# Kernel optimization log

Measured on AMD Instinct MI355X. Metric: run time of the kernel, lower is better.

Reference implementation:

```python
import jax, jax.numpy as jnp
import numpy as np

NUM_GROUPS = 8
EPS = 1e-5


def setup_inputs() -> dict:
    key = jax.random.key(0)
    ks = jax.random.split(key, 7)
    b, c, h, w = 4, 256, 64, 64
    x = jax.random.normal(ks[0], (b, c, h, w), dtype=jnp.float32)
    gamma = jnp.ones((c,), dtype=jnp.float32)
    beta = jnp.zeros((c,), dtype=jnp.float32)
    # 1x1 convs stored as [out_ch, in_ch] matrices
    w_qkv = jax.random.normal(ks[1], (3 * c, c), dtype=jnp.float32) * (1.0 / np.sqrt(c))
    b_qkv = jax.random.normal(ks[2], (3 * c,), dtype=jnp.float32) * 0.01
    # NOTE: original zero-inits proj; use small random weights so the op is non-trivial
    w_proj = jax.random.normal(ks[3], (c, c), dtype=jnp.float32) * (1.0 / np.sqrt(c))
    b_proj = jax.random.normal(ks[4], (c,), dtype=jnp.float32) * 0.01
    return {"x": x, "gamma": gamma, "beta": beta, "w_qkv": w_qkv,
            "b_qkv": b_qkv, "w_proj": w_proj, "b_proj": b_proj}


def _group_norm(x, gamma, beta):
    b, c, h, w = x.shape
    xg = x.reshape(b, NUM_GROUPS, c // NUM_GROUPS, h, w)
    mean = jnp.mean(xg, axis=(2, 3, 4), keepdims=True)
    var = jnp.var(xg, axis=(2, 3, 4), keepdims=True)
    xg = (xg - mean) * jax.lax.rsqrt(var + EPS)
    x = xg.reshape(b, c, h, w)
    return x * gamma[None, :, None, None] + beta[None, :, None, None]


def reference(x, gamma, beta, w_qkv, b_qkv, w_proj, b_proj):
    b, c, h, w = x.shape
    n = h * w
    residual = x
    xn = _group_norm(x, gamma, beta)
    # 1x1 conv qkv: [b, 3c, h, w]
    qkv = jnp.einsum('bchw,oc->bohw', xn, w_qkv) + b_qkv[None, :, None, None]
    q, k, v = jnp.split(qkv, 3, axis=1)
    q = q.reshape(b, c, n).transpose(0, 2, 1)   # [b, n, c]
    k = k.reshape(b, c, n)                       # [b, c, n]
    v = v.reshape(b, c, n).transpose(0, 2, 1)   # [b, n, c]
    scale = 1.0 / jnp.sqrt(jnp.asarray(c, dtype=x.dtype))
    attn = jnp.einsum('bic,bcj->bij', q, k) * scale    # [b, n, n]
    attn = jax.nn.softmax(attn, axis=-1)
    out = jnp.einsum('bij,bjc->bic', attn, v)          # [b, n, c]
    out = out.transpose(0, 2, 1).reshape(b, c, h, w)
    out = jnp.einsum('bchw,oc->bohw', out, w_proj) + b_proj[None, :, None, None]
    return out + residual
```

## Files before the change

### kernel.cpp

```cpp
#include <hip/hip_runtime.h>
#include <math.h>

#define BB   4
#define CC   256
#define NN   4096
#define GG   8
#define CPG  32
#define EPSV 1e-5f
#define SCALE 0.0625f
#define NSPLIT 4
#define PSTR 40

typedef __attribute__((ext_vector_type(8))) short bf16x8;
typedef __attribute__((ext_vector_type(4))) float f32x4;

struct alignas(8) us4 { unsigned short x, y, z, w; };

static __device__ __forceinline__ unsigned short f2bf(float f) {
    union { float f; unsigned int u; } a; a.f = f;
    unsigned int r = a.u + 0x7fffu + ((a.u >> 16) & 1u);
    return (unsigned short)(r >> 16);
}
static __device__ __forceinline__ void async16(const unsigned short* g, unsigned short* l) {
    __builtin_amdgcn_global_load_lds(
        (const __attribute__((address_space(1))) unsigned int*)g,
        (__attribute__((address_space(3))) unsigned int*)l,
        16, 0, 0);
}


__global__ __launch_bounds__(256) void prep_kernel(
    const float* __restrict__ x, const float* __restrict__ w_qkv,
    const float* __restrict__ w_proj, float* __restrict__ partials,
    unsigned short* __restrict__ wbf)
{
    const int tid = threadIdx.x;
    if (blockIdx.x >= 256) {
        int idx = ((blockIdx.x - 256)*256 + tid) * 4;
        float4 v;
        if (idx < 196608) v = *(const float4*)(w_qkv + idx);
        else              v = *(const float4*)(w_proj + (idx - 196608));
        us4 h = { f2bf(v.x), f2bf(v.y), f2bf(v.z), f2bf(v.w) };
        int o = idx >> 8, c = idx & 255;
        size_t dst = ((size_t)((o >> 4)*8 + (c >> 5)))*512
                   + ((((c & 31) >> 3))*16 + (o & 15))*8 + (c & 7);
        *(us4*)(wbf + dst) = h;
        return;
    }
    const int bg = blockIdx.x >> 3, slice = blockIdx.x & 7;
    const float4* base = (const float4*)(x + (size_t)bg*CPG*NN + slice*16384);
    float s = 0.f, sq = 0.f;
    for (int i = tid; i < 4096; i += 256) {
        float4 v = base[i];
        s  += v.x + v.y + v.z + v.w;
        sq += v.x*v.x + v.y*v.y + v.z*v.z + v.w*v.w;
    }
    __shared__ float ls[256], lq[256];
    ls[tid] = s; lq[tid] = sq;
    __syncthreads();
    for (int off = 128; off > 0; off >>= 1) {
        if (tid < off) { ls[tid] += ls[tid+off]; lq[tid] += lq[tid+off]; }
        __syncthreads();
    }
    if (tid == 0) { partials[blockIdx.x*2] = ls[0]; partials[blockIdx.x*2+1] = lq[0]; }
}

__global__ __launch_bounds__(256) void norm_t_kernel(
    const float* __restrict__ x, const float* __restrict__ gamma,
    const float* __restrict__ beta, const float* __restrict__ partials,
    unsigned short* __restrict__ xnT)
{
    const int n0 = blockIdx.x * 64;
    const int c0 = blockIdx.y * 64;
    const int b  = blockIdx.z;
    const int tid = threadIdx.x;
    __shared__ unsigned short T[64*68];
    __shared__ float ssc[64], ssh[64];
    if (tid < 64) {
        int c = c0 + tid;
        int bg = b*GG + (c >> 5);
        float s = 0.f, sq = 0.f;
        for (int i = 0; i < 8; i++) {
            s  += partials[(bg*8 + i)*2];
            sq += partials[(bg*8 + i)*2 + 1];
        }
        const float cnt = (float)(CPG*NN);
        float mean = s / cnt;
        float var  = sq / cnt - mean*mean;
        float rstd = rsqrtf(var + EPSV);
        float g = gamma[c], be = beta[c];
        ssc[tid] = rstd*g;
        ssh[tid] = be - mean*rstd*g;
    }
    __syncthreads();
    {
        int cl = tid >> 4, n4 = tid & 15;
        for (int i = 0; i < 4; i++) {
            int c = cl + i*16;
            float4 v = *(const float4*)(x + ((size_t)(b*CC + c0 + c))*NN + n0 + n4*4);
            float sc = ssc[c], sh = ssh[c];
            T[(n4*4+0)*68 + c] = f2bf(v.x*sc + sh);
            T[(n4*4+1)*68 + c] = f2bf(v.y*sc + sh);
            T[(n4*4+2)*68 + c] = f2bf(v.z*sc + sh);
            T[(n4*4+3)*68 + c] = f2bf(v.w*sc + sh);
        }
    }
    __syncthreads();
    {
        int nl = tid >> 3, cs = tid & 7;
        for (int i = 0; i < 2; i++) {
            int n = nl + i*32;
            int gg = (b*NN + n0 + n) >> 4;
            int kk = (c0 >> 5) + (cs >> 2);
            size_t dst = ((size_t)(gg*8 + kk))*512 + ((cs & 3)*16 + (n & 15))*8;
            *(bf16x8*)(xnT + dst) = *(const bf16x8*)&T[n*68 + cs*8];
        }
    }
}

__global__ __launch_bounds__(256, 3) void qkv_mfma_kernel(
    const unsigned short* __restrict__ xnT, const unsigned short* __restrict__ wbf,
    const float* __restrict__ b_qkv,
    unsigned short* __restrict__ qsw, unsigned short* __restrict__ ksw,
    unsigned short* __restrict__ vsw)
{
    const int tid  = threadIdx.x;
    const int wave = tid >> 6, lane = tid & 63;
    const int lrow = lane & 15, quad = lane >> 4;
    const int R0   = blockIdx.x * 128;
    const int b    = blockIdx.x >> 5;
    const int nb0  = (blockIdx.x & 31) * 128;
    const int oBase = blockIdx.y * 64;
    const int which = oBase >> 8;
    const int o0l   = oBase & 255;
    const bool isV  = (which == 2);
    const int wn = wave >> 1, wo = wave & 1;
    const int wg0 = oBase >> 4;

    __shared__ unsigned short lw[16384];
    __shared__ unsigned short lx[2][4096];

    const unsigned short* wsrc = wbf + ((size_t)(wg0 + wave))*8*512 + lane*8;
    for (int kk = 0; kk < 8; kk++)
        async16(wsrc + kk*512, lw + (wave*8 + kk)*512);
    const unsigned short* xsrc = xnT + (size_t)R0*CC + lane*8;
    for (int i = 0; i < 2; i++) {
        int g = wave*2 + i;
        async16(xsrc + (size_t)g*4096, lx[0] + g*512);
    }
    asm volatile("s_waitcnt vmcnt(0)" ::: "memory");
    __builtin_amdgcn_s_barrier();

    f32x4 acc[4][2];
    for (int s = 0; s < 4; s++) for (int t = 0; t < 2; t++)
        acc[s][t] = (f32x4){0.f, 0.f, 0.f, 0.f};

    for (int kk = 0; kk < 8; kk++) {
        const int cur = kk & 1, nxt = cur ^ 1;
        if (kk + 1 < 8) {
            for (int i = 0; i < 2; i++) {
                int g = wave*2 + i;
                async16(xsrc + (size_t)g*4096 + (kk+1)*512, lx[nxt] + g*512);
            }
        }
        bf16x8 af[4], bfr[2];
        if (!isV) {
            for (int s = 0; s < 4; s++)
                af[s]  = *(const bf16x8*)(lw + (s*8 + kk)*512 + lane*8);
            for (int t = 0; t < 2; t++)
                bfr[t] = *(const bf16x8*)(lx[cur] + (wave*2 + t)*512 + lane*8);
        } else {
            for (int s = 0; s < 4; s++)
                af[s]  = *(const bf16x8*)(lx[cur] + (wn*4 + s)*512 + lane*8);
            for (int t = 0; t < 2; t++)
                bfr[t] = *(const bf16x8*)(lw + ((wo*2 + t)*8 + kk)*512 + lane*8);
        }
        __builtin_amdgcn_s_setprio(1);
        for (int s = 0; s < 4; s++)
            for (int t = 0; t < 2; t++)
                acc[s][t] = __builtin_amdgcn_mfma_f32_16x16x32_bf16(af[s], bfr[t], acc[s][t], 0, 0, 0);
        __builtin_amdgcn_s_setprio(0);
        asm volatile("s_waitcnt vmcnt(0) lgkmcnt(0)" ::: "memory");
        __builtin_amdgcn_s_barrier();
    }

    unsigned short* lds = lw;

    if (!isV) {
        const float sc = (which == 0) ? SCALE : 1.0f;
        for (int s = 0; s < 4; s++) {
            float bias[4];
            for (int r = 0; r < 4; r++) bias[r] = b_qkv[oBase + s*16 + quad*4 + r];
            for (int t = 0; t < 2; t++) {
                us4 h;
                h.x = f2bf((acc[s][t][0] + bias[0]) * sc);
                h.y = f2bf((acc[s][t][1] + bias[1]) * sc);
                h.z = f2bf((acc[s][t][2] + bias[2]) * sc);
                h.w = f2bf((acc[s][t][3] + bias[3]) * sc);
                int chunk = (wave*2 + t)*2 + (s>>1);
                int pos = (((s*2 + (quad>>1)) & 3)*16 + lrow)*8 + (quad&1)*4;
                *(us4*)&lds[chunk*512 + pos] = h;
            }
        }
    } else {
        for (int s = 0; s < 4; s++)
            for (int t = 0; t < 2; t++) {
                int oc = o0l + wo*32 + t*16 + lrow;
                float bias = b_qkv[512 + oc];
                us4 h;
                h.x = f2bf(acc[s][t][0] + bias);
                h.y = f2bf(acc[s][t][1] + bias);
                h.z = f2bf(acc[s][t][2] + bias);
                h.w = f2bf(acc[s][t][3] + bias);
                int chunk = (wn*2 + (s>>1))*4 + wo*2 + t;
                int pos = (((s&1)*2 + (quad>>1))*16 + lrow)*8 + (quad&1)*4;
                *(us4*)&lds[chunk*512 + pos] = h;
            }
    }
    __syncthreads();

    if (!isV) {
        unsigned short* dst = (which == 0) ? qsw : ksw;
        for (int it = 0; it < 4; it++) {
            int f = it*4 + (tid>>6);
            int ng_l = f >> 1, kk_l = f & 1;
            size_t off = ((size_t)(b*256 + (nb0>>4) + ng_l)*8 + (o0l>>5) + kk_l)*512 + lane*8;
            *(bf16x8*)(dst + off) = *(const bf16x8*)&lds[f*512 + lane*8];
        }
    } else {
        for (int it = 0; it < 4; it++) {
            int f = it*4 + (tid>>6);
            int jg_l = f >> 2, ns_l = f & 3;
            size_t off = ((size_t)(b*128 + (nb0>>5) + jg_l)*16 + (o0l>>4) + ns_l)*512 + lane*8;
            *(bf16x8*)(vsw + off) = *(const bf16x8*)&lds[f*512 + lane*8];
        }
    }
}

__global__ __launch_bounds__(256, 2) void attn_mfma_kernel(
    const unsigned short* __restrict__ qsw, const unsigned short* __restrict__ ksw,
    const unsigned short* __restrict__ vsw,
    unsigned short* __restrict__ opart, float* __restrict__ lpart)
{
    const int tid  = threadIdx.x;
    const int wave = tid >> 6, lane = tid & 63;
    const int lrow = lane & 15, quad = lane >> 4;
    const int bx    = blockIdx.x;
    const int split = bx & 3;
    const int ig    = (bx >> 2) & 31;
    const int b     = bx >> 7;
    const int i0w   = ig*128 + wave*32;
    const int koff  = split * (NN / NSPLIT);
    const int NT    = (NN / NSPLIT) / 32;

    __shared__ unsigned short ldsK[2][8192];
    __shared__ unsigned short ldsV[2][8192];
    __shared__ unsigned short ldsP[4][32*PSTR];

    bf16x8 qf[2][8];
    {
        const unsigned short* qb = qsw + ((size_t)b << 20) + (size_t)i0w*256 + lane*8;
        for (int g = 0; g < 2; g++)
            for (int kk = 0; kk < 8; kk++)
                qf[g][kk] = *(const bf16x8*)(qb + g*4096 + kk*512);
    }

    f32x4 o_acc[2][16];
    for (int g = 0; g < 2; g++)
        for (int ns = 0; ns < 16; ns++)
            o_acc[g][ns] = (f32x4){0.f, 0.f, 0.f, 0.f};
    float lsum[2] = {0.f, 0.f};

    const unsigned short* kp = ksw + ((size_t)b << 20) + (size_t)koff*256 + wave*2048 + lane*8;
    const unsigned short* vp = vsw + ((size_t)b << 20) + (size_t)koff*256 + wave*2048 + lane*8;

    for (int t = 0; t < 4; t++) {
        async16(kp + t*512, ldsK[0] + wave*2048 + t*512);
        async16(vp + t*512, ldsV[0] + wave*2048 + t*512);
    }
    asm volatile("s_waitcnt vmcnt(0)" ::: "memory");
    __builtin_amdgcn_s_barrier();

    for (int jt = 0; jt < NT; jt++) {
        const int cur = jt & 1, nxt = cur ^ 1;

        if (jt + 1 < NT) {
            for (int t = 0; t < 4; t++) {
                async16(kp + (size_t)(jt+1)*8192 + t*512, ldsK[nxt] + wave*2048 + t*512);
                async16(vp + (size_t)(jt+1)*8192 + t*512, ldsV[nxt] + wave*2048 + t*512);
            }
        }

        f32x4 s[2][2];
        for (int jg = 0; jg < 2; jg++)
            for (int g = 0; g < 2; g++)
                s[jg][g] = (f32x4){0.f, 0.f, 0.f, 0.f};
        const unsigned short* lk = ldsK[cur];
        __builtin_amdgcn_s_setprio(1);
        for (int jg = 0; jg < 2; jg++)
            for (int kk = 0; kk < 8; kk++) {
                bf16x8 kf = *(const bf16x8*)(lk + (jg*8 + kk)*512 + lane*8);
                s[jg][0] = __builtin_amdgcn_mfma_f32_16x16x32_bf16(kf, qf[0][kk], s[jg][0], 0, 0, 0);
                s[jg][1] = __builtin_amdgcn_mfma_f32_16x16x32_bf16(kf, qf[1][kk], s[jg][1], 0, 0, 0);
            }
        __builtin_amdgcn_s_setprio(0);

        unsigned short* pw = ldsP[wave];
        for (int jg = 0; jg < 2; jg++)
            for (int g = 0; g < 2; g++) {
                float p0 = __expf(s[jg][g][0]);
                float p1 = __expf(s[jg][g][1]);
                float p2 = __expf(s[jg][g][2]);
                float p3 = __expf(s[jg][g][3]);
                lsum[g] += p0 + p1 + p2 + p3;
                us4 h = { f2bf(p0), f2bf(p1), f2bf(p2), f2bf(p3) };
                *(us4*)(pw + (g*16 + lrow)*PSTR + jg*16 + quad*4) = h;
            }

        bf16x8 pa[2];
        for (int g = 0; g < 2; g++)
            pa[g] = *(const bf16x8*)(pw + (g*16 + lrow)*PSTR + quad*8);

        const unsigned short* lv = ldsV[cur];
        __builtin_amdgcn_s_setprio(1);
        for (int ns = 0; ns < 16; ns++) {
            bf16x8 vf = *(const bf16x8*)(lv + ns*512 + lane*8);
            o_acc[0][ns] = __builtin_amdgcn_mfma_f32_16x16x32_bf16(pa[0], vf, o_acc[0][ns], 0, 0, 0);
            o_acc[1][ns] = __builtin_amdgcn_mfma_f32_16x16x32_bf16(pa[1], vf, o_acc[1][ns], 0, 0, 0);
        }
        __builtin_amdgcn_s_setprio(0);

        asm volatile("s_waitcnt vmcnt(0) lgkmcnt(0)" ::: "memory");
        __builtin_amdgcn_s_barrier();
    }

    for (int g = 0; g < 2; g++) {
        float v = lsum[g];
        v += __shfl_xor(v, 16);
        v += __shfl_xor(v, 32);
        lsum[g] = v;
    }

    unsigned short* reg = &ldsV[0][0] + wave*4096;
    const size_t planeb = ((size_t)(split*BB + b)) << 20;
    for (int g = 0; g < 2; g++) {
        for (int ns = 0; ns < 16; ns++) {
            int kk = ns >> 1;
            int posbase = ((ns & 1)*2 + (lrow >> 3))*128 + (lrow & 7) + quad*32;
            for (int r = 0; r < 4; r++)
                reg[kk*512 + posbase + r*8] = f2bf(o_acc[g][ns][r]);
        }
        unsigned short* dst = opart + planeb + ((size_t)((i0w >> 4) + g))*4096;
        for (int kk = 0; kk < 8; kk++)
            *(bf16x8*)(dst + kk*512 + lane*8) = *(const bf16x8*)(reg + kk*512 + lane*8);
    }
    if (quad == 0)
        for (int g = 0; g < 2; g++)
            lpart[(size_t)(split*BB + b)*NN + i0w + g*16 + lrow] = lsum[g];
}

__global__ __launch_bounds__(256, 4) void proj_mfma_kernel(
    const unsigned short* __restrict__ opart, const float* __restrict__ lpart,
    const unsigned short* __restrict__ w2bf, const float* __restrict__ b_proj,
    const float* __restrict__ x, float* __restrict__ out)
{
    const int tid  = threadIdx.x;
    const int wave = tid >> 6, lane = tid & 63;
    const int lrow = lane & 15, quad = lane >> 4;
    const int rt = blockIdx.x & 255;
    const int oq = blockIdx.x >> 8;
    const int b  = rt >> 6;
    const int n0 = (rt & 63) * 64;

    const int rg = (n0 >> 4) + wave;
    const unsigned short* Ab = opart + ((size_t)b << 20) + (size_t)rg*4096 + lane*8;
    const size_t pstride = (size_t)BB << 20;

    __shared__ unsigned short la[2][8192];

    for (int sp = 0; sp < NSPLIT; sp++)
        async16(Ab + (size_t)sp*pstride, la[0] + (wave*4 + sp)*512);
    asm volatile("s_waitcnt vmcnt(0)" ::: "memory");

    f32x4 acc[4];
    for (int t = 0; t < 4; t++) acc[t] = (f32x4){0.f, 0.f, 0.f, 0.f};

    for (int kk = 0; kk < 8; kk++) {
        const int cur = kk & 1, nxt = cur ^ 1;
        if (kk + 1 < 8)
            for (int sp = 0; sp < NSPLIT; sp++)
                async16(Ab + (size_t)sp*pstride + (kk+1)*512, la[nxt] + (wave*4 + sp)*512);

        bf16x8 bfr[4];
        for (int t = 0; t < 4; t++)
            bfr[t] = *(const bf16x8*)(w2bf + ((size_t)((oq*4 + t)*8 + kk))*512 + lane*8);

        __builtin_amdgcn_s_setprio(1);
        for (int sp = 0; sp < NSPLIT; sp++) {
            bf16x8 af = *(const bf16x8*)(la[cur] + (wave*4 + sp)*512 + lane*8);
            for (int t = 0; t < 4; t++)
                acc[t] = __builtin_amdgcn_mfma_f32_16x16x32_bf16(af, bfr[t], acc[t], 0, 0, 0);
        }
        __builtin_amdgcn_s_setprio(0);

        asm volatile("s_waitcnt vmcnt(0)" ::: "memory");
    }

    float sinv[4];
    for (int r = 0; r < 4; r++) {
        int n = n0 + wave*16 + quad*4 + r;
        float l = 0.f;
        for (int sp = 0; sp < NSPLIT; sp++)
            l += lpart[(size_t)(sp*BB + b)*NN + n];
        sinv[r] = 1.0f / l;
    }

    for (int t = 0; t < 4; t++) {
        int o = oq*64 + t*16 + lrow;
        int n = n0 + wave*16 + quad*4;
        size_t idx = ((size_t)(b*CC + o))*NN + n;
        float bias = b_proj[o];
        float4 xv = *(const float4*)(x + idx);
        float4 ov;
        ov.x = acc[t][0]*sinv[0] + bias + xv.x;
        ov.y = acc[t][1]*sinv[1] + bias + xv.y;
        ov.z = acc[t][2]*sinv[2] + bias + xv.z;
        ov.w = acc[t][3]*sinv[3] + bias + xv.w;
        *(float4*)(out + idx) = ov;
    }
}

extern "C" void kernel_launch(void* const* d_in, const int* in_sizes, int n_in,
                              void* d_out, int out_size, void* d_ws, size_t ws_size,
                              hipStream_t stream) {
    const float* x      = (const float*)d_in[0];
    const float* gamma  = (const float*)d_in[1];
    const float* beta   = (const float*)d_in[2];
    const float* w_qkv  = (const float*)d_in[3];
    const float* b_qkv  = (const float*)d_in[4];
    const float* w_proj = (const float*)d_in[5];
    const float* b_proj = (const float*)d_in[6];
    float* out = (float*)d_out;

    const size_t plane = (size_t)BB * NN * CC;
    unsigned short* xnT = (unsigned short*)d_ws;
    unsigned short* qsw = xnT + plane;
    unsigned short* ksw = qsw + plane;
    unsigned short* vsw = ksw + plane;
    unsigned short* wbf = vsw + plane;
    unsigned short* opart = wbf + 262144;
    float* lpart    = (float*)(opart + (size_t)NSPLIT*plane);
    float* partials = lpart + (size_t)NSPLIT*BB*NN;

    prep_kernel<<<512, 256, 0, stream>>>(x, w_qkv, w_proj, partials, wbf);

    dim3 gnt(64, 4, BB);
    norm_t_kernel<<<gnt, 256, 0, stream>>>(x, gamma, beta, partials, xnT);

    dim3 gq(128, 12);
    qkv_mfma_kernel<<<gq, 256, 0, stream>>>(xnT, wbf, b_qkv, qsw, ksw, vsw);

    attn_mfma_kernel<<<BB*32*NSPLIT, 256, 0, stream>>>(qsw, ksw, vsw, opart, lpart);

    proj_mfma_kernel<<<1024, 256, 0, stream>>>(opart, lpart, wbf + 196608, b_proj, x, out);
}
```

Before: 190.4 us.

## Fuse all stages into one cooperative persistent kernel with grid syncs

Merges the five stage kernels (group-norm stats, normalize/transpose, QKV GEMM, attention, projection) into a single cooperative kernel of 512 blocks. Stages are separated by grid.sync(), and each stage iterates virtual block ids over the persistent grid. Shared memory becomes one statically sized buffer carved per phase. The aim is to remove kernel launch gaps and tail effects between stages. In exchange, every block reserves the largest phase's LDS and the fused kernel runs at a single occupancy and register budget, which may hurt the QKV and proj phases that previously ran at higher occupancy. If the cooperative launch fails, it falls back to separate launches.

```diff
diff --git a/kernel.cpp b/kernel.cpp
--- a/kernel.cpp
+++ b/kernel.cpp
@@ -1,5 +1,8 @@
 #include <hip/hip_runtime.h>
+#include <hip/hip_cooperative_groups.h>
 #include <math.h>
+
+namespace cg = cooperative_groups;
 
 #define BB   4
 #define CC   256
@@ -10,6 +13,7 @@
 #define SCALE 0.0625f
 #define NSPLIT 4
 #define PSTR 40
+#define SMEM_BYTES 75776
 
 typedef __attribute__((ext_vector_type(8))) short bf16x8;
 typedef __attribute__((ext_vector_type(4))) float f32x4;
@@ -29,14 +33,13 @@
 }
 
 
-__global__ __launch_bounds__(256) void prep_kernel(
+static __device__ void prep_phase(int vb, int tid, char* smem,
     const float* __restrict__ x, const float* __restrict__ w_qkv,
     const float* __restrict__ w_proj, float* __restrict__ partials,
     unsigned short* __restrict__ wbf)
 {
-    const int tid = threadIdx.x;
-    if (blockIdx.x >= 256) {
-        int idx = ((blockIdx.x - 256)*256 + tid) * 4;
+    if (vb >= 256) {
+        int idx = ((vb - 256)*256 + tid) * 4;
         float4 v;
         if (idx < 196608) v = *(const float4*)(w_qkv + idx);
         else              v = *(const float4*)(w_proj + (idx - 196608));
@@ -47,7 +50,7 @@
         *(us4*)(wbf + dst) = h;
         return;
     }
-    const int bg = blockIdx.x >> 3, slice = blockIdx.x & 7;
+    const int bg = vb >> 3, slice = vb & 7;
     const float4* base = (const float4*)(x + (size_t)bg*CPG*NN + slice*16384);
     float s = 0.f, sq = 0.f;
     for (int i = tid; i < 4096; i += 256) {
@@ -55,27 +58,28 @@
         s  += v.x + v.y + v.z + v.w;
         sq += v.x*v.x + v.y*v.y + v.z*v.z + v.w*v.w;
     }
-    __shared__ float ls[256], lq[256];
+    float* ls = (float*)smem;
+    float* lq = ls + 256;
     ls[tid] = s; lq[tid] = sq;
     __syncthreads();
     for (int off = 128; off > 0; off >>= 1) {
         if (tid < off) { ls[tid] += ls[tid+off]; lq[tid] += lq[tid+off]; }
         __syncthreads();
     }
-    if (tid == 0) { partials[blockIdx.x*2] = ls[0]; partials[blockIdx.x*2+1] = lq[0]; }
-}
-
-__global__ __launch_bounds__(256) void norm_t_kernel(
+    if (tid == 0) { partials[vb*2] = ls[0]; partials[vb*2+1] = lq[0]; }
+}
+
+static __device__ void norm_phase(int vb, int tid, char* smem,
     const float* __restrict__ x, const float* __restrict__ gamma,
     const float* __restrict__ beta, const float* __restrict__ partials,
     unsigned short* __restrict__ xnT)
 {
-    const int n0 = blockIdx.x * 64;
-    const int c0 = blockIdx.y * 64;
-    const int b  = blockIdx.z;
-    const int tid = threadIdx.x;
-    __shared__ unsigned short T[64*68];
-    __shared__ float ssc[64], ssh[64];
+    const int n0 = (vb & 63) * 64;
+    const int c0 = ((vb >> 6) & 3) * 64;
+    const int b  = vb >> 8;
+    unsigned short* T = (unsigned short*)smem;
+    float* ssc = (float*)(smem + 8704);
+    float* ssh = (float*)(smem + 8960);
     if (tid < 64) {
         int c = c0 + tid;
         int bg = b*GG + (c >> 5);
@@ -118,27 +122,29 @@
     }
 }
 
-__global__ __launch_bounds__(256, 3) void qkv_mfma_kernel(
+static __device__ void qkv_phase(int vb, int tid, char* smem,
     const unsigned short* __restrict__ xnT, const unsigned short* __restrict__ wbf,
     const float* __restrict__ b_qkv,
     unsigned short* __restrict__ qsw, unsigned short* __restrict__ ksw,
     unsigned short* __restrict__ vsw)
 {
-    const int tid  = threadIdx.x;
     const int wave = tid >> 6, lane = tid & 63;
     const int lrow = lane & 15, quad = lane >> 4;
-    const int R0   = blockIdx.x * 128;
-    const int b    = blockIdx.x >> 5;
-    const int nb0  = (blockIdx.x & 31) * 128;
-    const int oBase = blockIdx.y * 64;
+    const int bxx  = vb & 127;
+    const int R0   = bxx * 128;
+    const int b    = bxx >> 5;
+    const int nb0  = (bxx & 31) * 128;
+    const int oBase = (vb >> 7) * 64;
     const int which = oBase >> 8;
     const int o0l   = oBase & 255;
     const bool isV  = (which == 2);
     const int wn = wave >> 1, wo = wave & 1;
     const int wg0 = oBase >> 4;
 
-    __shared__ unsigned short lw[16384];
-    __shared__ unsigned short lx[2][4096];
+    unsigned short* lw = (unsigned short*)smem;
+    unsigned short* lx0 = (unsigned short*)(smem + 32768);
+    unsigned short* lx1 = (unsigned short*)(smem + 40960);
+    unsigned short* lxx[2] = { lx0, lx1 };
 
     const unsigned short* wsrc = wbf + ((size_t)(wg0 + wave))*8*512 + lane*8;
     for (int kk = 0; kk < 8; kk++)
@@ -146,7 +152,7 @@
     const unsigned short* xsrc = xnT + (size_t)R0*CC + lane*8;
     for (int i = 0; i < 2; i++) {
         int g = wave*2 + i;
-        async16(xsrc + (size_t)g*4096, lx[0] + g*512);
+        async16(xsrc + (size_t)g*4096, lx0 + g*512);
     }
     asm volatile("s_waitcnt vmcnt(0)" ::: "memory");
     __builtin_amdgcn_s_barrier();
@@ -160,7 +166,7 @@
         if (kk + 1 < 8) {
             for (int i = 0; i < 2; i++) {
                 int g = wave*2 + i;
-                async16(xsrc + (size_t)g*4096 + (kk+1)*512, lx[nxt] + g*512);
+                async16(xsrc + (size_t)g*4096 + (kk+1)*512, lxx[nxt] + g*512);
             }
         }
         bf16x8 af[4], bfr[2];
@@ -168,10 +174,10 @@
             for (int s = 0; s < 4; s++)
                 af[s]  = *(const bf16x8*)(lw + (s*8 + kk)*512 + lane*8);
             for (int t = 0; t < 2; t++)
-                bfr[t] = *(const bf16x8*)(lx[cur] + (wave*2 + t)*512 + lane*8);
+                bfr[t] = *(const bf16x8*)(lxx[cur] + (wave*2 + t)*512 + lane*8);
         } else {
             for (int s = 0; s < 4; s++)
-                af[s]  = *(const bf16x8*)(lx[cur] + (wn*4 + s)*512 + lane*8);
+                af[s]  = *(const bf16x8*)(lxx[cur] + (wn*4 + s)*512 + lane*8);
             for (int t = 0; t < 2; t++)
                 bfr[t] = *(const bf16x8*)(lw + ((wo*2 + t)*8 + kk)*512 + lane*8);
         }
@@ -237,15 +243,13 @@
     }
 }
 
-__global__ __launch_bounds__(256, 2) void attn_mfma_kernel(
+static __device__ void attn_phase(int bx, int tid, char* smem,
     const unsigned short* __restrict__ qsw, const unsigned short* __restrict__ ksw,
     const unsigned short* __restrict__ vsw,
     unsigned short* __restrict__ opart, float* __restrict__ lpart)
 {
-    const int tid  = threadIdx.x;
     const int wave = tid >> 6, lane = tid & 63;
     const int lrow = lane & 15, quad = lane >> 4;
-    const int bx    = blockIdx.x;
     const int split = bx & 3;
     const int ig    = (bx >> 2) & 31;
     const int b     = bx >> 7;
@@ -253,9 +257,13 @@
     const int koff  = split * (NN / NSPLIT);
     const int NT    = (NN / NSPLIT) / 32;
 
-    __shared__ unsigned short ldsK[2][8192];
-    __shared__ unsigned short ldsV[2][8192];
-    __shared__ unsigned short ldsP[4][32*PSTR];
+    unsigned short* ldsK0 = (unsigned short*)smem;
+    unsigned short* ldsK1 = (unsigned short*)(smem + 16384);
+    unsigned short* ldsV0 = (unsigned short*)(smem + 32768);
+    unsigned short* ldsV1 = (unsigned short*)(smem + 49152);
+    unsigned short* ldsP  = (unsigned short*)(smem + 65536);
+    unsigned short* ldsKb[2] = { ldsK0, ldsK1 };
+    unsigned short* ldsVb[2] = { ldsV0, ldsV1 };
 
     bf16x8 qf[2][8];
     {
@@ -275,8 +283,8 @@
     const unsigned short* vp = vsw + ((size_t)b << 20) + (size_t)koff*256 + wave*2048 + lane*8;
 
     for (int t = 0; t < 4; t++) {
-        async16(kp + t*512, ldsK[0] + wave*2048 + t*512);
-        async16(vp + t*512, ldsV[0] + wave*2048 + t*512);
+        async16(kp + t*512, ldsK0 + wave*2048 + t*512);
+        async16(vp + t*512, ldsV0 + wave*2048 + t*512);
     }
     asm volatile("s_waitcnt vmcnt(0)" ::: "memory");
     __builtin_amdgcn_s_barrier();
@@ -286,8 +294,8 @@
 
         if (jt + 1 < NT) {
             for (int t = 0; t < 4; t++) {
-                async16(kp + (size_t)(jt+1)*8192 + t*512, ldsK[nxt] + wave*2048 + t*512);
-                async16(vp + (size_t)(jt+1)*8192 + t*512, ldsV[nxt] + wave*2048 + t*512);
+                async16(kp + (size_t)(jt+1)*8192 + t*512, ldsKb[nxt] + wave*2048 + t*512);
+                async16(vp + (size_t)(jt+1)*8192 + t*512, ldsVb[nxt] + wave*2048 + t*512);
             }
         }
 
@@ -295,7 +303,7 @@
         for (int jg = 0; jg < 2; jg++)
             for (int g = 0; g < 2; g++)
                 s[jg][g] = (f32x4){0.f, 0.f, 0.f, 0.f};
-        const unsigned short* lk = ldsK[cur];
+        const unsigned short* lk = ldsKb[cur];
         __builtin_amdgcn_s_setprio(1);
         for (int jg = 0; jg < 2; jg++)
             for (int kk = 0; kk < 8; kk++) {
@@ -305,7 +313,7 @@
             }
         __builtin_amdgcn_s_setprio(0);
 
-        unsigned short* pw = ldsP[wave];
+        unsigned short* pw = ldsP + wave*32*PSTR;
         for (int jg = 0; jg < 2; jg++)
             for (int g = 0; g < 2; g++) {
                 float p0 = __expf(s[jg][g][0]);
@@ -321,7 +329,7 @@
         for (int g = 0; g < 2; g++)
             pa[g] = *(const bf16x8*)(pw + (g*16 + lrow)*PSTR + quad*8);
 
-        const unsigned short* lv = ldsV[cur];
+        const unsigned short* lv = ldsVb[cur];
         __builtin_amdgcn_s_setprio(1);
         for (int ns = 0; ns < 16; ns++) {
             bf16x8 vf = *(const bf16x8*)(lv + ns*512 + lane*8);
@@ -341,7 +349,7 @@
         lsum[g] = v;
     }
 
-    unsigned short* reg = &ldsV[0][0] + wave*4096;
+    unsigned short* reg = ldsV0 + wave*4096;
     const size_t planeb = ((size_t)(split*BB + b)) << 20;
     for (int g = 0; g < 2; g++) {
         for (int ns = 0; ns < 16; ns++) {
@@ -359,16 +367,15 @@
             lpart[(size_t)(split*BB + b)*NN + i0w + g*16 + lrow] = lsum[g];
 }
 
-__global__ __launch_bounds__(256, 4) void proj_mfma_kernel(
+static __device__ void proj_phase(int vb, int tid, char* smem,
     const unsigned short* __restrict__ opart, const float* __restrict__ lpart,
     const unsigned short* __restrict__ w2bf, const float* __restrict__ b_proj,
     const float* __restrict__ x, float* __restrict__ out)
 {
-    const int tid  = threadIdx.x;
     const int wave = tid >> 6, lane = tid & 63;
     const int lrow = lane & 15, quad = lane >> 4;
-    const int rt = blockIdx.x & 255;
-    const int oq = blockIdx.x >> 8;
+    const int rt = vb & 255;
+    const int oq = vb >> 8;
     const int b  = rt >> 6;
     const int n0 = (rt & 63) * 64;
 
@@ -376,10 +383,12 @@
     const unsigned short* Ab = opart + ((size_t)b << 20) + (size_t)rg*4096 + lane*8;
     const size_t pstride = (size_t)BB << 20;
 
-    __shared__ unsigned short la[2][8192];
+    unsigned short* la0 = (unsigned short*)smem;
+    unsigned short* la1 = (unsigned short*)(smem + 16384);
+    unsigned short* lab[2] = { la0, la1 };
 
     for (int sp = 0; sp < NSPLIT; sp++)
-        async16(Ab + (size_t)sp*pstride, la[0] + (wave*4 + sp)*512);
+        async16(Ab + (size_t)sp*pstride, la0 + (wave*4 + sp)*512);
     asm volatile("s_waitcnt vmcnt(0)" ::: "memory");
 
     f32x4 acc[4];
@@ -389,7 +398,7 @@
         const int cur = kk & 1, nxt = cur ^ 1;
         if (kk + 1 < 8)
             for (int sp = 0; sp < NSPLIT; sp++)
-                async16(Ab + (size_t)sp*pstride + (kk+1)*512, la[nxt] + (wave*4 + sp)*512);
+                async16(Ab + (size_t)sp*pstride + (kk+1)*512, lab[nxt] + (wave*4 + sp)*512);
 
         bf16x8 bfr[4];
         for (int t = 0; t < 4; t++)
@@ -397,7 +406,7 @@
 
         __builtin_amdgcn_s_setprio(1);
         for (int sp = 0; sp < NSPLIT; sp++) {
-            bf16x8 af = *(const bf16x8*)(la[cur] + (wave*4 + sp)*512 + lane*8);
+            bf16x8 af = *(const bf16x8*)(lab[cur] + (wave*4 + sp)*512 + lane*8);
             for (int t = 0; t < 4; t++)
                 acc[t] = __builtin_amdgcn_mfma_f32_16x16x32_bf16(af, bfr[t], acc[t], 0, 0, 0);
         }
@@ -430,6 +439,93 @@
     }
 }
 
+__global__ __launch_bounds__(256, 2) void fused_kernel(
+    const float* x, const float* gamma, const float* beta,
+    const float* w_qkv, const float* b_qkv, const float* w_proj,
+    const float* b_proj, float* out, unsigned short* ws)
+{
+    __shared__ __align__(16) char smem[SMEM_BYTES];
+    const int bid = blockIdx.x, tid = threadIdx.x;
+    cg::grid_group grid = cg::this_grid();
+
+    const size_t plane = (size_t)BB * NN * CC;
+    unsigned short* xnT = ws;
+    unsigned short* qsw = xnT + plane;
+    unsigned short* ksw = qsw + plane;
+    unsigned short* vsw = ksw + plane;
+    unsigned short* wbf = vsw + plane;
+    unsigned short* opart = wbf + 262144;
+    float* lpart    = (float*)(opart + (size_t)NSPLIT*plane);
+    float* partials = lpart + (size_t)NSPLIT*BB*NN;
+
+    prep_phase(bid, tid, smem, x, w_qkv, w_proj, partials, wbf);
+    grid.sync();
+
+    for (int v = bid; v < 1024; v += 512) {
+        __syncthreads();
+        norm_phase(v, tid, smem, x, gamma, beta, partials, xnT);
+    }
+    grid.sync();
+
+    for (int v = bid; v < 1536; v += 512) {
+        __syncthreads();
+        qkv_phase(v, tid, smem, xnT, wbf, b_qkv, qsw, ksw, vsw);
+    }
+    grid.sync();
+
+    attn_phase(bid, tid, smem, qsw, ksw, vsw, opart, lpart);
+    grid.sync();
+
+    for (int v = bid; v < 1024; v += 512)
+        proj_phase(v, tid, smem, opart, lpart, wbf + 196608, b_proj, x, out);
+}
+
+__global__ __launch_bounds__(256) void prep_kernel(
+    const float* __restrict__ x, const float* __restrict__ w_qkv,
+    const float* __restrict__ w_proj, float* __restrict__ partials,
+    unsigned short* __restrict__ wbf)
+{
+    __shared__ __align__(16) char smem[2048];
+    prep_phase(blockIdx.x, threadIdx.x, smem, x, w_qkv, w_proj, partials, wbf);
+}
+
+__global__ __launch_bounds__(256) void norm_t_kernel(
+    const float* __restrict__ x, const float* __restrict__ gamma,
+    const float* __restrict__ beta, const float* __restrict__ partials,
+    unsigned short* __restrict__ xnT)
+{
+    __shared__ __align__(16) char smem[9216];
+    norm_phase(blockIdx.x, threadIdx.x, smem, x, gamma, beta, partials, xnT);
+}
+
+__global__ __launch_bounds__(256, 3) void qkv_mfma_kernel(
+    const unsigned short* __restrict__ xnT, const unsigned short* __restrict__ wbf,
+    const float* __restrict__ b_qkv,
+    unsigned short* __restrict__ qsw, unsigned short* __restrict__ ksw,
+    unsigned short* __restrict__ vsw)
+{
+    __shared__ __align__(16) char smem[49152];
+    qkv_phase(blockIdx.x, threadIdx.x, smem, xnT, wbf, b_qkv, qsw, ksw, vsw);
+}
+
+__global__ __launch_bounds__(256, 2) void attn_mfma_kernel(
+    const unsigned short* __restrict__ qsw, const unsigned short* __restrict__ ksw,
+    const unsigned short* __restrict__ vsw,
+    unsigned short* __restrict__ opart, float* __restrict__ lpart)
+{
+    __shared__ __align__(16) char smem[SMEM_BYTES];
+    attn_phase(blockIdx.x, threadIdx.x, smem, qsw, ksw, vsw, opart, lpart);
+}
+
+__global__ __launch_bounds__(256, 4) void proj_mfma_kernel(
+    const unsigned short* __restrict__ opart, const float* __restrict__ lpart,
+    const unsigned short* __restrict__ w2bf, const float* __restrict__ b_proj,
+    const float* __restrict__ x, float* __restrict__ out)
+{
+    __shared__ __align__(16) char smem[32768];
+    proj_phase(blockIdx.x, threadIdx.x, smem, opart, lpart, w2bf, b_proj, x, out);
+}
+
 extern "C" void kernel_launch(void* const* d_in, const int* in_sizes, int n_in,
                               void* d_out, int out_size, void* d_ws, size_t ws_size,
                               hipStream_t stream) {
@@ -441,26 +537,30 @@
     const float* w_proj = (const float*)d_in[5];
     const float* b_proj = (const float*)d_in[6];
     float* out = (float*)d_out;
-
-    const size_t plane = (size_t)BB * NN * CC;
-    unsigned short* xnT = (unsigned short*)d_ws;
-    unsigned short* qsw = xnT + plane;
-    unsigned short* ksw = qsw + plane;
-    unsigned short* vsw = ksw + plane;
-    unsigned short* wbf = vsw + plane;
-    unsigned short* opart = wbf + 262144;
-    float* lpart    = (float*)(opart + (size_t)NSPLIT*plane);
-    float* partials = lpart + (size_t)NSPLIT*BB*NN;
-
-    prep_kernel<<<512, 256, 0, stream>>>(x, w_qkv, w_proj, partials, wbf);
-
-    dim3 gnt(64, 4, BB);
-    norm_t_kernel<<<gnt, 256, 0, stream>>>(x, gamma, beta, partials, xnT);
-
-    dim3 gq(128, 12);
-    qkv_mfma_kernel<<<gq, 256, 0, stream>>>(xnT, wbf, b_qkv, qsw, ksw, vsw);
-
-    attn_mfma_kernel<<<BB*32*NSPLIT, 256, 0, stream>>>(qsw, ksw, vsw, opart, lpart);
-
-    proj_mfma_kernel<<<1024, 256, 0, stream>>>(opart, lpart, wbf + 196608, b_proj, x, out);
-}
+    unsigned short* ws = (unsigned short*)d_ws;
+
+    void* kargs[] = { (void*)&x, (void*)&gamma, (void*)&beta, (void*)&w_qkv,
+                      (void*)&b_qkv, (void*)&w_proj, (void*)&b_proj,
+                      (void*)&out, (void*)&ws };
+    hipError_t err = hipLaunchCooperativeKernel(
+        (const void*)fused_kernel, dim3(512), dim3(256), kargs, 0, stream);
+
+    if (err != hipSuccess) {
+        (void)hipGetLastError();
+        const size_t plane = (size_t)BB * NN * CC;
+        unsigned short* xnT = ws;
+        unsigned short* qsw = xnT + plane;
+        unsigned short* ksw = qsw + plane;
+        unsigned short* vsw = ksw + plane;
+        unsigned short* wbf = vsw + plane;
+        unsigned short* opart = wbf + 262144;
+        float* lpart    = (float*)(opart + (size_t)NSPLIT*plane);
+        float* partials = lpart + (size_t)NSPLIT*BB*NN;
+
+        prep_kernel<<<512, 256, 0, stream>>>(x, w_qkv, w_proj, partials, wbf);
+        norm_t_kernel<<<1024, 256, 0, stream>>>(x, gamma, beta, partials, xnT);
+        qkv_mfma_kernel<<<1536, 256, 0, stream>>>(xnT, wbf, b_qkv, qsw, ksw, vsw);
+        attn_mfma_kernel<<<512, 256, 0, stream>>>(qsw, ksw, vsw, opart, lpart);
+        proj_mfma_kernel<<<1024, 256, 0, stream>>>(opart, lpart, wbf + 196608, b_proj, x, out);
+    }
+}
```

Measured after the change: 457.0 us. 140% more time.
